# Kernel optimization log

Measured on AMD Instinct MI355X. Metric: run time of the kernel, lower is better.

The kernel has to match this reference:

```python
import jax, jax.numpy as jnp
import numpy as np

NUM_HEADS = 16
B, S, D = 2, 2048, 1024


def setup_inputs() -> dict:
    key = jax.random.key(0)
    ks = jax.random.split(key, 6)
    return {
        "q": jax.random.normal(ks[0], (B, S, D), dtype=jnp.float32),
        "k": jax.random.normal(ks[1], (B, S, D), dtype=jnp.float32),
        "v": jax.random.normal(ks[2], (B, S, D), dtype=jnp.float32),
        "wq": jax.random.normal(ks[3], (D, D), dtype=jnp.float32) * (1.0 / np.sqrt(D)),
        "wk": jax.random.normal(ks[4], (D, D), dtype=jnp.float32) * (1.0 / np.sqrt(D)),
        "wv": jax.random.normal(ks[5], (D, D), dtype=jnp.float32) * (1.0 / np.sqrt(D)),
    }


def reference(q, k, v, wq, wk, wv):
    b, s, d = q.shape
    h = NUM_HEADS
    hd = d // h

    def proj(x, w):
        # torch Linear (no bias): x @ w.T ; chunk(dim=2) == reshape to heads
        return (x @ w.T).reshape(b, s, h, hd).transpose(0, 2, 1, 3)  # [b,h,s,hd]

    qh, kh, vh = proj(q, wq), proj(k, wk), proj(v, wv)
    scale = 1.0 / jnp.sqrt(jnp.asarray(hd, q.dtype))
    scores = jnp.einsum("bhqd,bhkd->bhqk", qh, kh) * scale  # [b,h,s,s]
    # faithful to torch: .tril() zeroes (not -inf) the upper triangle pre-softmax
    mask = jnp.tril(jnp.ones((s, s), dtype=bool))
    scores = jnp.where(mask, scores, jnp.asarray(0.0, scores.dtype))
    attn = jax.nn.softmax(scores, axis=-1)
    out = jnp.einsum("bhqk,bhkd->bhqd", attn, vh)  # [b,h,s,hd]
    return out.transpose(0, 2, 1, 3).reshape(b, s, d)
```

## Files before the change

### kernel.cpp

```cpp
#include <hip/hip_runtime.h>
#include <math.h>

#define B_  2
#define S_  2048
#define D_  1024
#define H_  16
#define HD_ 64
#define NT_ (S_/64)
#define C2_ (0.125f * 1.44269504088896f)

typedef __attribute__((ext_vector_type(8))) _Float16 f16x8;
typedef __attribute__((ext_vector_type(2))) __fp16 h16x2;
typedef __attribute__((ext_vector_type(4))) float f32x4;
typedef unsigned short u16;
typedef unsigned int   u32;

__device__ inline u16 f2h(float f) {
    union { _Float16 h; u16 u; } c; c.h = (_Float16)f;
    return c.u;
}
__device__ inline u32 pkrtz(float a, float b) {
    union { h16x2 h; u32 u; } c;
    c.h = __builtin_amdgcn_cvt_pkrtz(a, b);
    return c.u;
}

#define GLOAD_LDS16(g, l)                                                    \
    __builtin_amdgcn_global_load_lds(                                        \
        (const __attribute__((address_space(1))) void*)(g),                  \
        (__attribute__((address_space(3))) void*)(l), 16, 0, 0)

__global__ __launch_bounds__(256)
void precast(const float* __restrict__ wq, const float* __restrict__ wk,
             const float* __restrict__ wv, const float* __restrict__ q,
             const float* __restrict__ k,  const float* __restrict__ v,
             u16* __restrict__ Wq, u16* __restrict__ Wk, u16* __restrict__ Wv,
             u16* __restrict__ Xq, u16* __restrict__ Xk, u16* __restrict__ Xv)
{
    const int z = blockIdx.y;
    const size_t n = (z >= 3) ? (size_t)B_ * S_ * D_ : (size_t)D_ * D_;
    const size_t i = ((size_t)blockIdx.x * 256 + threadIdx.x) * 4;
    if (i >= n) return;
    const float* src = (z == 0) ? wq : (z == 1) ? wk : (z == 2) ? wv
                     : (z == 3) ? q  : (z == 4) ? k  : v;
    u16* dst = (z == 0) ? Wq : (z == 1) ? Wk : (z == 2) ? Wv
             : (z == 3) ? Xq : (z == 4) ? Xk : Xv;
    float4 xv = *(const float4*)&src[i];
    *(ushort4*)&dst[i] = make_ushort4(f2h(xv.x), f2h(xv.y), f2h(xv.z), f2h(xv.w));
}

__global__ __launch_bounds__(256, 2)
void proj_all(const u16* __restrict__ Xq, const u16* __restrict__ Xk,
              const u16* __restrict__ Xv, const u16* __restrict__ Wq,
              const u16* __restrict__ Wk, const u16* __restrict__ Wv,
              u16* __restrict__ QP, u16* __restrict__ KP, u16* __restrict__ VT)
{
    const int bid = (int)blockIdx.x;
    const int g   = (bid & 7) * 96 + (bid >> 3);
    const int z   = g >> 8;
    const int rem = g & 255;
    const int ny  = rem >> 3;
    const int nx  = rem & 7;

    const u16* X = (z == 0) ? Xq : (z == 1) ? Xk : Xv;
    const u16* W = (z == 0) ? Wq : (z == 1) ? Wk : Wv;

    __shared__ u16 Xs[2][128 * 64];
    __shared__ u16 Ws[2][128 * 64];

    const int tid  = threadIdx.x;
    const int w    = tid >> 6;
    const int lane = tid & 63;
    const int quad = lane >> 4;
    const int lr   = lane & 15;
    const int wm   = w >> 1;
    const int wn   = w & 1;
    const int m0   = ny * 128;
    const int n0   = nx * 128;

    const int srow  = w * 32 + (lane >> 3);
    const int gslot = (lane & 7) ^ ((lane >> 3) & 7);
    const size_t xbase = (size_t)(m0 + srow) * D_ + gslot * 8;
    const size_t wbase = (size_t)(n0 + srow) * D_ + gslot * 8;
    const int ldsoff = w * 2048 + lane * 8;

    f32x4 acc[4][4];
    #pragma unroll
    for (int i = 0; i < 4; ++i)
        #pragma unroll
        for (int j = 0; j < 4; ++j) acc[i][j] = (f32x4){0.f, 0.f, 0.f, 0.f};

    #pragma unroll
    for (int c = 0; c < 4; ++c) {
        GLOAD_LDS16(X + xbase + (size_t)c * 8 * D_, &Xs[0][ldsoff + c * 512]);
        GLOAD_LDS16(W + wbase + (size_t)c * 8 * D_, &Ws[0][ldsoff + c * 512]);
    }

    for (int t = 0; t < 16; ++t) {
        const int cur = t & 1;
        if (t < 15) {
            const size_t ko = (size_t)(t + 1) * 64;
            #pragma unroll
            for (int c = 0; c < 4; ++c) {
                GLOAD_LDS16(X + xbase + (size_t)c * 8 * D_ + ko,
                            &Xs[cur ^ 1][ldsoff + c * 512]);
                GLOAD_LDS16(W + wbase + (size_t)c * 8 * D_ + ko,
                            &Ws[cur ^ 1][ldsoff + c * 512]);
            }
            asm volatile("s_waitcnt vmcnt(8)" ::: "memory");
        } else {
            asm volatile("s_waitcnt vmcnt(0)" ::: "memory");
        }
        __builtin_amdgcn_s_barrier();

        f16x8 bf[4][2], af[4][2];
        #pragma unroll
        for (int fn = 0; fn < 4; ++fn) {
            const int row = wn * 64 + fn * 16 + lr;
            #pragma unroll
            for (int kk = 0; kk < 2; ++kk)
                bf[fn][kk] = *(const f16x8*)
                    &Ws[cur][row * 64 + (((kk * 4 + quad) ^ (lr & 7)) << 3)];
        }
        #pragma unroll
        for (int fm = 0; fm < 4; ++fm) {
            const int row = wm * 64 + fm * 16 + lr;
            #pragma unroll
            for (int kk = 0; kk < 2; ++kk)
                af[fm][kk] = *(const f16x8*)
                    &Xs[cur][row * 64 + (((kk * 4 + quad) ^ (lr & 7)) << 3)];
        }
        #pragma unroll
        for (int fm = 0; fm < 4; ++fm)
            #pragma unroll
            for (int fn = 0; fn < 4; ++fn)
                #pragma unroll
                for (int kk = 0; kk < 2; ++kk)
                    acc[fm][fn] = __builtin_amdgcn_mfma_f32_16x16x32_f16(
                        af[fm][kk], bf[fn][kk], acc[fm][fn], 0, 0, 0);
        __builtin_amdgcn_s_barrier();
    }

    if (z < 2) {
        u16* P = (z == 0) ? QP : KP;
        const float sc = (z == 0) ? C2_ : 1.0f;
        #pragma unroll
        for (int fm = 0; fm < 4; ++fm)
            #pragma unroll
            for (int fn = 0; fn < 4; ++fn) {
                int n = n0 + wn * 64 + fn * 16 + lr;
                int h = n >> 6, hd = n & 63;
                #pragma unroll
                for (int r = 0; r < 4; ++r) {
                    int m = m0 + wm * 64 + fm * 16 + quad * 4 + r;
                    int b = m >> 11, s = m & (S_ - 1);
                    P[(((size_t)b * H_ + h) * S_ + s) * HD_ + hd] =
                        f2h(acc[fm][fn][r] * sc);
                }
            }
    } else {
        #pragma unroll
        for (int fm = 0; fm < 4; ++fm)
            #pragma unroll
            for (int fn = 0; fn < 4; ++fn) {
                int n  = n0 + wn * 64 + fn * 16 + lr;
                int h  = n >> 6, vd = n & 63;
                int m  = m0 + wm * 64 + fm * 16 + quad * 4;
                int b  = m >> 11, s = m & (S_ - 1);
                ushort4 pv = make_ushort4(f2h(acc[fm][fn][0]), f2h(acc[fm][fn][1]),
                                          f2h(acc[fm][fn][2]), f2h(acc[fm][fn][3]));
                *(ushort4*)&VT[(((size_t)b * H_ + h) * HD_ + vd) * S_ + s] = pv;
            }
    }
}

__global__ __launch_bounds__(64)
void vtilesum_kernel(const u16* __restrict__ VT, float* __restrict__ TS)
{
    const int t = blockIdx.x, bh = blockIdx.y, vd = threadIdx.x;
    const u16* p = VT + ((size_t)bh * HD_ + vd) * S_ + t * 64;
    float acc = 0.f;
    #pragma unroll
    for (int c = 0; c < 8; ++c) {
        f16x8 vv = *(const f16x8*)&p[c * 8];
        #pragma unroll
        for (int j = 0; j < 8; ++j) acc += (float)vv[j];
    }
    TS[((size_t)bh * NT_ + t) * HD_ + vd] = acc;
}

__global__ __launch_bounds__(64)
void vsuffix_kernel(const float* __restrict__ TS, float* __restrict__ SUF)
{
    const int bh = blockIdx.x, c = threadIdx.x;
    float acc = 0.f;
    SUF[((size_t)bh * (NT_ + 1) + NT_) * HD_ + c] = 0.f;
    for (int t = NT_ - 1; t >= 0; --t) {
        acc += TS[((size_t)bh * NT_ + t) * HD_ + c];
        SUF[((size_t)bh * (NT_ + 1) + t) * HD_ + c] = acc;
    }
}

__global__ __launch_bounds__(256)
void attn_mfma(const u16* __restrict__ QP, const u16* __restrict__ KP,
               const u16* __restrict__ VT, const float* __restrict__ SUF,
               float* __restrict__ OUT)
{
    const int bh = blockIdx.x;
    const int tq = NT_ - 1 - (int)blockIdx.y;
    const int b  = bh >> 4, h = bh & 15;

    __shared__ u16 Ks[64 * 64];
    __shared__ u16 Vth[64 * 64];
    __shared__ u16 Phi[4 * 16 * 64];

    const int tid  = threadIdx.x;
    const int w    = tid >> 6;
    const int lane = tid & 63;
    const int quad = lane >> 4;
    const int lr   = lane & 15;
    const int r    = tid >> 2;
    const int q4   = tid & 3;

    const u16* Qb = QP + (size_t)bh * S_ * HD_;
    const u16* Kb = KP + (size_t)bh * S_ * HD_;
    const u16* Vb = VT + (size_t)bh * HD_ * S_;

    const int q0 = tq * 64;

    f16x8 qf[2];
    #pragma unroll
    for (int ch = 0; ch < 2; ++ch)
        qf[ch] = *(const f16x8*)(Qb + (size_t)(q0 + w * 16 + lr) * HD_ +
                                 ch * 32 + quad * 8);

    f32x4 of[4];
    #pragma unroll
    for (int n = 0; n < 4; ++n) of[n] = (f32x4){0.f, 0.f, 0.f, 0.f};
    float l_i = 0.f;

    int soff[2];
    #pragma unroll
    for (int c = 0; c < 2; ++c)
        soff[c] = r * 64 + (((q4 * 2 + c) ^ (r & 7)) << 3);

    f16x8 kpre[2], vpre[2];
    #pragma unroll
    for (int c = 0; c < 2; ++c) {
        kpre[c] = *(const f16x8*)(Kb + (size_t)r * HD_ + q4 * 16 + c * 8);
        vpre[c] = *(const f16x8*)(Vb + (size_t)r * S_ + q4 * 16 + c * 8);
    }

    for (int t = 0; t <= tq; ++t) {
        const int k0t = t * 64;
        __syncthreads();
        #pragma unroll
        for (int c = 0; c < 2; ++c) {
            *(f16x8*)&Ks[soff[c]]  = kpre[c];
            *(f16x8*)&Vth[soff[c]] = vpre[c];
        }
        __syncthreads();
        if (t < tq) {
            const int kn = k0t + 64;
            #pragma unroll
            for (int c = 0; c < 2; ++c) {
                kpre[c] = *(const f16x8*)(Kb + (size_t)(kn + r) * HD_ + q4 * 16 + c * 8);
                vpre[c] = *(const f16x8*)(Vb + (size_t)r * S_ + kn + q4 * 16 + c * 8);
            }
        }

        f32x4 sf[4];
        #pragma unroll
        for (int f = 0; f < 4; ++f) sf[f] = (f32x4){0.f, 0.f, 0.f, 0.f};
        #pragma unroll
        for (int ch = 0; ch < 2; ++ch)
            #pragma unroll
            for (int f = 0; f < 4; ++f) {
                f16x8 ak = *(const f16x8*)
                    &Ks[(f * 16 + lr) * 64 + (((ch * 4 + quad) ^ (lr & 7)) << 3)];
                sf[f] = __builtin_amdgcn_mfma_f32_16x16x32_f16(ak, qf[ch], sf[f], 0, 0, 0);
            }

        if (t == tq) {
            const int ig = q0 + w * 16 + lr;
            #pragma unroll
            for (int f = 0; f < 4; ++f)
                #pragma unroll
                for (int i = 0; i < 4; ++i) {
                    int jg = k0t + f * 16 + quad * 4 + i;
                    sf[f][i] = (jg <= ig) ? sf[f][i] : 0.f;
                }
        }

        float ps = 0.f;
        #pragma unroll
        for (int f = 0; f < 4; ++f)
            #pragma unroll
            for (int i = 0; i < 4; ++i) {
                float p = exp2f(sf[f][i]);
                sf[f][i] = p;
                ps += p;
            }
        ps += __shfl_xor(ps, 16);
        ps += __shfl_xor(ps, 32);
        l_i += ps;

        #pragma unroll
        for (int f = 0; f < 4; ++f) {
            uint2 pw = make_uint2(pkrtz(sf[f][0], sf[f][1]),
                                  pkrtz(sf[f][2], sf[f][3]));
            *(uint2*)&Phi[(w * 16 + lr) * 64 +
                          (((f * 2 + (quad >> 1)) ^ (lr & 7)) << 3) +
                          (quad & 1) * 4] = pw;
        }

        #pragma unroll
        for (int ch = 0; ch < 2; ++ch) {
            f16x8 pb = *(const f16x8*)
                &Phi[(w * 16 + lr) * 64 + (((ch * 4 + quad) ^ (lr & 7)) << 3)];
            #pragma unroll
            for (int n = 0; n < 4; ++n) {
                f16x8 av = *(const f16x8*)
                    &Vth[(n * 16 + lr) * 64 + (((ch * 4 + quad) ^ (lr & 7)) << 3)];
                of[n] = __builtin_amdgcn_mfma_f32_16x16x32_f16(av, pb, of[n], 0, 0, 0);
            }
        }
    }

    const int cnt = S_ - (q0 + 64);
    const float* suf = SUF + ((size_t)bh * (NT_ + 1) + (tq + 1)) * HD_;
    float inv = 1.0f / (l_i + (float)cnt);
    const int srow = q0 + w * 16 + lr;
    #pragma unroll
    for (int n = 0; n < 4; ++n) {
        float4 sv = *(const float4*)&suf[n * 16 + quad * 4];
        float4 ov;
        ov.x = (of[n][0] + sv.x) * inv;
        ov.y = (of[n][1] + sv.y) * inv;
        ov.z = (of[n][2] + sv.z) * inv;
        ov.w = (of[n][3] + sv.w) * inv;
        *(float4*)&OUT[((size_t)b * S_ + srow) * D_ + h * HD_ + n * 16 + quad * 4] = ov;
    }
}

extern "C" void kernel_launch(void* const* d_in, const int* in_sizes, int n_in,
                              void* d_out, int out_size, void* d_ws, size_t ws_size,
                              hipStream_t stream)
{
    (void)in_sizes; (void)n_in; (void)out_size; (void)ws_size;
    const float* q  = (const float*)d_in[0];
    const float* k  = (const float*)d_in[1];
    const float* v  = (const float*)d_in[2];
    const float* wq = (const float*)d_in[3];
    const float* wk = (const float*)d_in[4];
    const float* wv = (const float*)d_in[5];
    float* out = (float*)d_out;

    const size_t PROJ = (size_t)B_ * H_ * S_ * HD_;
    const size_t WSZ  = (size_t)D_ * D_;
    u16* QP = (u16*)d_ws;
    u16* KP = QP + PROJ;
    u16* VT = KP + PROJ;
    u16* Xq = VT + PROJ;
    u16* Xk = Xq + PROJ;
    u16* Xv = Xk + PROJ;
    u16* Wq = Xv + PROJ;
    u16* Wk = Wq + WSZ;
    u16* Wv = Wk + WSZ;
    float* TS  = (float*)(Wv + WSZ);
    float* SUF = TS + (size_t)B_ * H_ * NT_ * HD_;

    precast<<<dim3(PROJ / 1024, 6), 256, 0, stream>>>(
        wq, wk, wv, q, k, v, Wq, Wk, Wv, Xq, Xk, Xv);
    proj_all<<<dim3(3 * (D_ / 128) * ((B_ * S_) / 128)), 256, 0, stream>>>(
        Xq, Xk, Xv, Wq, Wk, Wv, QP, KP, VT);
    vtilesum_kernel<<<dim3(NT_, B_ * H_), 64, 0, stream>>>(VT, TS);
    vsuffix_kernel<<<B_ * H_, 64, 0, stream>>>(TS, SUF);
    attn_mfma<<<dim3(B_ * H_, NT_), 256, 0, stream>>>(QP, KP, VT, SUF, out);
}
```

Before: 187.0 us.

## Double-buffer K/V tiles in attention and fuse V suffix-sum kernels

The attention kernel now keeps two LDS buffers for K and V tiles. The next tile is written into the alternate buffer before the current one is computed, which removes one __syncthreads per iteration and overlaps global loads with MFMA work. Separately, the V tile-sum and suffix-scan kernels are merged into one kernel that holds tile sums in shared memory, saving a launch and a global round trip. In exchange, LDS use per block doubles for K/V, which may lower occupancy. The fused kernel runs only 32 blocks, so it may have little parallelism.

```diff
diff --git a/kernel.cpp b/kernel.cpp
--- a/kernel.cpp
+++ b/kernel.cpp
@@ -174,30 +174,36 @@
     }
 }
 
-__global__ __launch_bounds__(64)
-void vtilesum_kernel(const u16* __restrict__ VT, float* __restrict__ TS)
-{
-    const int t = blockIdx.x, bh = blockIdx.y, vd = threadIdx.x;
-    const u16* p = VT + ((size_t)bh * HD_ + vd) * S_ + t * 64;
-    float acc = 0.f;
-    #pragma unroll
-    for (int c = 0; c < 8; ++c) {
-        f16x8 vv = *(const f16x8*)&p[c * 8];
-        #pragma unroll
-        for (int j = 0; j < 8; ++j) acc += (float)vv[j];
-    }
-    TS[((size_t)bh * NT_ + t) * HD_ + vd] = acc;
-}
-
-__global__ __launch_bounds__(64)
-void vsuffix_kernel(const float* __restrict__ TS, float* __restrict__ SUF)
-{
-    const int bh = blockIdx.x, c = threadIdx.x;
-    float acc = 0.f;
-    SUF[((size_t)bh * (NT_ + 1) + NT_) * HD_ + c] = 0.f;
-    for (int t = NT_ - 1; t >= 0; --t) {
-        acc += TS[((size_t)bh * NT_ + t) * HD_ + c];
-        SUF[((size_t)bh * (NT_ + 1) + t) * HD_ + c] = acc;
+__global__ __launch_bounds__(256)
+void vsum_kernel(const u16* __restrict__ VT, float* __restrict__ SUF)
+{
+    const int bh  = blockIdx.x;
+    const int tid = threadIdx.x;
+    __shared__ float TSs[NT_][HD_];
+
+    #pragma unroll
+    for (int i = 0; i < 8; ++i) {
+        const int task = i * 256 + tid;
+        const int t  = task >> 6;
+        const int vd = task & 63;
+        const u16* p = VT + ((size_t)bh * HD_ + vd) * S_ + t * 64;
+        float acc = 0.f;
+        #pragma unroll
+        for (int c = 0; c < 8; ++c) {
+            f16x8 vv = *(const f16x8*)&p[c * 8];
+            #pragma unroll
+            for (int j = 0; j < 8; ++j) acc += (float)vv[j];
+        }
+        TSs[t][vd] = acc;
+    }
+    __syncthreads();
+    if (tid < 64) {
+        float acc = 0.f;
+        SUF[((size_t)bh * (NT_ + 1) + NT_) * HD_ + tid] = 0.f;
+        for (int t = NT_ - 1; t >= 0; --t) {
+            acc += TSs[t][tid];
+            SUF[((size_t)bh * (NT_ + 1) + t) * HD_ + tid] = acc;
+        }
     }
 }
 
@@ -210,8 +216,8 @@
     const int tq = NT_ - 1 - (int)blockIdx.y;
     const int b  = bh >> 4, h = bh & 15;
 
-    __shared__ u16 Ks[64 * 64];
-    __shared__ u16 Vth[64 * 64];
+    __shared__ u16 Ks[2][64 * 64];
+    __shared__ u16 Vth[2][64 * 64];
     __shared__ u16 Phi[4 * 16 * 64];
 
     const int tid  = threadIdx.x;
@@ -250,22 +256,35 @@
         kpre[c] = *(const f16x8*)(Kb + (size_t)r * HD_ + q4 * 16 + c * 8);
         vpre[c] = *(const f16x8*)(Vb + (size_t)r * S_ + q4 * 16 + c * 8);
     }
+    #pragma unroll
+    for (int c = 0; c < 2; ++c) {
+        *(f16x8*)&Ks[0][soff[c]]  = kpre[c];
+        *(f16x8*)&Vth[0][soff[c]] = vpre[c];
+    }
+    if (tq >= 1) {
+        #pragma unroll
+        for (int c = 0; c < 2; ++c) {
+            kpre[c] = *(const f16x8*)(Kb + (size_t)(64 + r) * HD_ + q4 * 16 + c * 8);
+            vpre[c] = *(const f16x8*)(Vb + (size_t)r * S_ + 64 + q4 * 16 + c * 8);
+        }
+    }
 
     for (int t = 0; t <= tq; ++t) {
-        const int k0t = t * 64;
-        __syncthreads();
-        #pragma unroll
-        for (int c = 0; c < 2; ++c) {
-            *(f16x8*)&Ks[soff[c]]  = kpre[c];
-            *(f16x8*)&Vth[soff[c]] = vpre[c];
-        }
+        const int cb = t & 1;
         __syncthreads();
         if (t < tq) {
-            const int kn = k0t + 64;
             #pragma unroll
             for (int c = 0; c < 2; ++c) {
-                kpre[c] = *(const f16x8*)(Kb + (size_t)(kn + r) * HD_ + q4 * 16 + c * 8);
-                vpre[c] = *(const f16x8*)(Vb + (size_t)r * S_ + kn + q4 * 16 + c * 8);
+                *(f16x8*)&Ks[cb ^ 1][soff[c]]  = kpre[c];
+                *(f16x8*)&Vth[cb ^ 1][soff[c]] = vpre[c];
+            }
+            if (t + 2 <= tq) {
+                const int kn = (t + 2) * 64;
+                #pragma unroll
+                for (int c = 0; c < 2; ++c) {
+                    kpre[c] = *(const f16x8*)(Kb + (size_t)(kn + r) * HD_ + q4 * 16 + c * 8);
+                    vpre[c] = *(const f16x8*)(Vb + (size_t)r * S_ + kn + q4 * 16 + c * 8);
+                }
             }
         }
 
@@ -277,7 +296,7 @@
             #pragma unroll
             for (int f = 0; f < 4; ++f) {
                 f16x8 ak = *(const f16x8*)
-                    &Ks[(f * 16 + lr) * 64 + (((ch * 4 + quad) ^ (lr & 7)) << 3)];
+                    &Ks[cb][(f * 16 + lr) * 64 + (((ch * 4 + quad) ^ (lr & 7)) << 3)];
                 sf[f] = __builtin_amdgcn_mfma_f32_16x16x32_f16(ak, qf[ch], sf[f], 0, 0, 0);
             }
 
@@ -287,7 +306,7 @@
             for (int f = 0; f < 4; ++f)
                 #pragma unroll
                 for (int i = 0; i < 4; ++i) {
-                    int jg = k0t + f * 16 + quad * 4 + i;
+                    int jg = t * 64 + f * 16 + quad * 4 + i;
                     sf[f][i] = (jg <= ig) ? sf[f][i] : 0.f;
                 }
         }
@@ -321,7 +340,7 @@
             #pragma unroll
             for (int n = 0; n < 4; ++n) {
                 f16x8 av = *(const f16x8*)
-                    &Vth[(n * 16 + lr) * 64 + (((ch * 4 + quad) ^ (lr & 7)) << 3)];
+                    &Vth[cb][(n * 16 + lr) * 64 + (((ch * 4 + quad) ^ (lr & 7)) << 3)];
                 of[n] = __builtin_amdgcn_mfma_f32_16x16x32_f16(av, pb, of[n], 0, 0, 0);
             }
         }
@@ -367,14 +386,12 @@
     u16* Wq = Xv + PROJ;
     u16* Wk = Wq + WSZ;
     u16* Wv = Wk + WSZ;
-    float* TS  = (float*)(Wv + WSZ);
-    float* SUF = TS + (size_t)B_ * H_ * NT_ * HD_;
+    float* SUF = (float*)(Wv + WSZ);
 
     precast<<<dim3(PROJ / 1024, 6), 256, 0, stream>>>(
         wq, wk, wv, q, k, v, Wq, Wk, Wv, Xq, Xk, Xv);
     proj_all<<<dim3(3 * (D_ / 128) * ((B_ * S_) / 128)), 256, 0, stream>>>(
         Xq, Xk, Xv, Wq, Wk, Wv, QP, KP, VT);
-    vtilesum_kernel<<<dim3(NT_, B_ * H_), 64, 0, stream>>>(VT, TS);
-    vsuffix_kernel<<<B_ * H_, 64, 0, stream>>>(TS, SUF);
+    vsum_kernel<<<B_ * H_, 256, 0, stream>>>(VT, SUF);
     attn_mfma<<<dim3(B_ * H_, NT_), 256, 0, stream>>>(QP, KP, VT, SUF, out);
 }
```

New measurement: 194.2 us. 1.04x slower.
